# Kernel optimization log

Measured on AMD Instinct MI355X. Metric: run time of the kernel, lower is better.

## Reference

```python
import jax, jax.numpy as jnp
import numpy as np


def setup_inputs() -> dict:
    key = jax.random.key(0)
    k_cb, k_mask, k_y, k_yt, k_ym = jax.random.split(key, 5)
    B, L, M = 8, 2048, 4096
    CB = jax.random.normal(k_cb, (B, L, 3), dtype=jnp.float32) * 10.0
    # residue validity mask: mostly valid, some padding
    mask = (jax.random.uniform(k_mask, (B, L)) > 0.1).astype(jnp.float32)
    Y = jax.random.normal(k_y, (B, M, 3), dtype=jnp.float32) * 10.0
    Y_t = jax.random.randint(k_yt, (B, M), 0, 64, dtype=jnp.int32)
    Y_m = jax.random.randint(k_ym, (B, M), 0, 2, dtype=jnp.int32)
    return {"CB": CB, "mask": mask, "Y": Y, "Y_t": Y_t, "Y_m": Y_m,
            "number_of_ligand_atoms": 25}


def reference(CB, mask, Y, Y_t, Y_m, number_of_ligand_atoms):
    # CB: [B, L, 3], mask: [B, L], Y: [B, M, 3], Y_t/Y_m: [B, M]
    B, L, _ = CB.shape
    k = number_of_ligand_atoms
    Y_m_f = Y_m.astype(jnp.float32)
    mask_CBY = mask[:, :, None] * Y_m_f[:, None, :]          # [B, L, M]
    d = CB[:, :, None, :] - Y[:, None, :, :]                 # [B, L, M, 3]
    L2_AB = jnp.sum(d * d, axis=-1)                          # [B, L, M]
    L2_AB = L2_AB * mask_CBY + (1.0 - mask_CBY) * 1000.0
    # k smallest distances per (b, l); torch uses full argsort + slice,
    # top_k of the negated matrix selects the same set.
    neg_vals, nn_idx = jax.lax.top_k(-L2_AB, k)              # [B, L, k]
    L2_AB_nn = -neg_vals
    D_AB_closest = jnp.sqrt(L2_AB_nn[:, :, 0])               # [B, L]
    b_idx = jnp.arange(B)[:, None, None]                     # [B, 1, 1]
    Y_out = Y[b_idx, nn_idx]                                 # [B, L, k, 3]
    Y_t_out = Y_t[b_idx, nn_idx].astype(jnp.int32)           # [B, L, k]
    Y_m_out = Y_m[b_idx, nn_idx].astype(jnp.int32)           # [B, L, k]
    return Y_out, Y_t_out, Y_m_out, D_AB_closest
```

## Files before the change

kernel.cpp:

```cpp
#include <hip/hip_runtime.h>

#pragma clang fp contract(off)

typedef unsigned long long u64;
typedef unsigned int u32;
typedef unsigned short u16;
typedef float f32x2 __attribute__((ext_vector_type(2)));

#define BB 8
#define LL 2048
#define MM 4096
#define KK 25
#define WPB 16
#define TPB 1024
#define CAP 3072
#define SENT  0xFFFFFFFFFFFFFFFFull
#define SENTH 0xFFFFFFFFu

static __device__ __forceinline__ u32 wave_min_u32(u32 x) {
    u32 t;
    t = (u32)__builtin_amdgcn_update_dpp(0, (int)x, 0xB1, 0xF, 0xF, true);
    x = t < x ? t : x;
    t = (u32)__builtin_amdgcn_update_dpp(0, (int)x, 0x4E, 0xF, 0xF, true);
    x = t < x ? t : x;
    t = (u32)__builtin_amdgcn_update_dpp(0, (int)x, 0x141, 0xF, 0xF, true);
    x = t < x ? t : x;
    t = (u32)__builtin_amdgcn_update_dpp(0, (int)x, 0x140, 0xF, 0xF, true);
    x = t < x ? t : x;
    t = (u32)__builtin_amdgcn_update_dpp((int)x, (int)x, 0x142, 0xF, 0xF, false);
    x = t < x ? t : x;
    t = (u32)__builtin_amdgcn_update_dpp((int)x, (int)x, 0x143, 0xF, 0xF, false);
    x = t < x ? t : x;
    return (u32)__builtin_amdgcn_readlane((int)x, 63);
}

__global__ void __launch_bounds__(TPB, 8) knn_kernel(
    const float* __restrict__ CB, const float* __restrict__ maskA,
    const float* __restrict__ Y, const int* __restrict__ Yt,
    const int* __restrict__ Ym, float* __restrict__ out)
{
    __shared__ __align__(16) float sX[CAP];
    __shared__ __align__(16) float sY[CAP];
    __shared__ __align__(16) float sZ[CAP];
    __shared__ u16 sP16[CAP];
    __shared__ u16 sMidx[64];
    __shared__ int sWinc[16];
    __shared__ int sWbase[16];
    __shared__ int sVtot;
    __shared__ u64 sExt[WPB][64];
    __shared__ u64 sR[WPB][KK];

    const int tid  = threadIdx.x;
    const int lane = tid & 63;
    const int wv   = tid >> 6;
    const int blk  = blockIdx.x;
    const int b    = blk >> 7;
    const int qg   = blk & 127;

    const float* Yb  = Y  + (size_t)b * MM * 3;
    const int*   Ymb = Ym + (size_t)b * MM;
    const int*   Ytb = Yt + (size_t)b * MM;

    const int p0 = tid << 2;
    const float4 f0 = *(const float4*)(Yb + 3 * p0);
    const float4 f1 = *(const float4*)(Yb + 3 * p0 + 4);
    const float4 f2 = *(const float4*)(Yb + 3 * p0 + 8);
    const int4   m4 = *(const int4*)(Ymb + p0);
    const int v0 = (m4.x != 0), v1 = (m4.y != 0), v2 = (m4.z != 0), v3 = (m4.w != 0);
    const int cnt0 = v0 + v1 + v2 + v3;

    int inc = cnt0;
#pragma unroll
    for (int off = 1; off < 64; off <<= 1) {
        const int t = __shfl_up(inc, off, 64);
        if (lane >= off) inc += t;
    }
    if (lane == 63) sWinc[wv] = inc;
    __syncthreads();
    if (tid < 16) {
        const int x = sWinc[tid];
        int ix = x;
#pragma unroll
        for (int off = 1; off < 16; off <<= 1) {
            const int t = __shfl_up(ix, off, 16);
            if (tid >= off) ix += t;
        }
        sWbase[tid] = ix - x;
        if (tid == 15) sVtot = ix;
    }
    __syncthreads();

    {
        int bs = sWbase[wv] + inc - cnt0;
        int mb = p0 - bs;
        if (v0) { sX[bs]=f0.x; sY[bs]=f0.y; sZ[bs]=f0.z; sP16[bs]=(u16)(p0+0); bs++; }
        else    { if (mb < 64) sMidx[mb] = (u16)(p0 + 0); mb++; }
        if (v1) { sX[bs]=f0.w; sY[bs]=f1.x; sZ[bs]=f1.y; sP16[bs]=(u16)(p0+1); bs++; }
        else    { if (mb < 64) sMidx[mb] = (u16)(p0 + 1); mb++; }
        if (v2) { sX[bs]=f1.z; sY[bs]=f1.w; sZ[bs]=f2.x; sP16[bs]=(u16)(p0+2); bs++; }
        else    { if (mb < 64) sMidx[mb] = (u16)(p0 + 2); mb++; }
        if (v3) { sX[bs]=f2.y; sY[bs]=f2.z; sZ[bs]=f2.w; sP16[bs]=(u16)(p0+3); bs++; }
        else    { if (mb < 64) sMidx[mb] = (u16)(p0 + 3); mb++; }
    }
    const int V  = sVtot;
    const int NJ = (V + 255) >> 8;
    for (int c = V + tid; c < (NJ << 8); c += TPB) {
        sX[c] = __builtin_inff(); sY[c] = 0.0f; sZ[c] = 0.0f; sP16[c] = 4095;
    }
    __syncthreads();

    const int l = qg * WPB + wv;
    const int q = b * LL + l;

    float* out_y = out;
    float* out_t = out + (size_t)BB * LL * KK * 3;
    float* out_m = out_t + (size_t)BB * LL * KK;
    float* out_d = out_m + (size_t)BB * LL * KK;

    if (maskA[q] == 0.0f) {
        if (lane < KK) {
            const int p = lane;
            const size_t o = (size_t)q * KK + lane;
            out_y[3 * o + 0] = Yb[3 * p + 0];
            out_y[3 * o + 1] = Yb[3 * p + 1];
            out_y[3 * o + 2] = Yb[3 * p + 2];
            out_t[o] = (float)Ytb[p];
            out_m[o] = (float)Ymb[p];
            if (lane == 0) out_d[q] = sqrtf(1000.0f);
        }
        return;
    }

    const float cx = CB[3 * q + 0];
    const float cy = CB[3 * q + 1];
    const float cz = CB[3 * q + 2];

    float v1f = 3.0e38f, v2f = 3.0e38f, v3f = 3.0e38f, v4f = 3.0e38f;
    u32 J = 0u;
    const u32 SEL1 = 0x06050400u;
    const u32 SEL2 = 0x06050004u;
    const u32 SEL3 = 0x06000504u;
    const u32 SEL4 = 0x00060504u;
    auto ins = [&](float v, u32 id) {
        const bool c1 = v < v1f, c2 = v < v2f, c3 = v < v3f, c4 = v < v4f;
        const u32 sel = c1 ? SEL1 : (c2 ? SEL2 : (c3 ? SEL3 : SEL4));
        const u32 Jp  = __builtin_amdgcn_perm(J, id, sel);
        const float n2 = __builtin_amdgcn_fmed3f(v, v1f, v2f);
        const float n3 = __builtin_amdgcn_fmed3f(v, v2f, v3f);
        const float n4 = __builtin_amdgcn_fmed3f(v, v3f, v4f);
        v1f = fminf(v, v1f);
        v2f = n2; v3f = n3; v4f = n4;
        J = c4 ? Jp : J;
    };

    const f32x2 cxx = {cx, cx}, cyy = {cy, cy}, czz = {cz, cz};
#pragma unroll 2
    for (int j = 0; j < NJ; ++j) {
        const int base = (j << 8) + (lane << 2);
        const float4 xq = *(const float4*)&sX[base];
        const float4 yq = *(const float4*)&sY[base];
        const float4 zq = *(const float4*)&sZ[base];
        f32x2 dx = cxx - f32x2{xq.x, xq.y};
        f32x2 dy = cyy - f32x2{yq.x, yq.y};
        f32x2 dz = czz - f32x2{zq.x, zq.y};
        const f32x2 d01 = (dx * dx + dy * dy) + dz * dz;
        dx = cxx - f32x2{xq.z, xq.w};
        dy = cyy - f32x2{yq.z, yq.w};
        dz = czz - f32x2{zq.z, zq.w};
        const f32x2 d23 = (dx * dx + dy * dy) + dz * dz;
        ins(d01.x, (u32)(j << 2));
        ins(d01.y, (u32)((j << 2) | 1));
        ins(d23.x, (u32)((j << 2) | 2));
        ins(d23.y, (u32)((j << 2) | 3));
    }

    auto slotof = [&](u32 id) -> u32 {
        return ((id >> 2) << 8) | (u32)(lane << 2) | (id & 3u);
    };

    const u32 s1 = slotof( J        & 0xFFu);
    const u32 s2 = slotof((J >>  8) & 0xFFu);
    const u32 s3 = slotof((J >> 16) & 0xFFu);
    const u32 s4 = slotof((J >> 24) & 0xFFu);
    u32 h1 = __float_as_uint(v1f) + 1u;
    u32 h2 = __float_as_uint(v2f) + 1u;
    u32 h3 = __float_as_uint(v3f) + 1u;
    u32 h4 = __float_as_uint(v4f) + 1u;
    u64 lref = ((u64)h4 << 32) | s4;

    bool fb = false;
    u64 myk = 0;
    {
        const u32 T = wave_min_u32(h4);
        const bool c1 = (h1 <= T), c2 = (h2 <= T), c3 = (h3 <= T), c4 = (h4 <= T);
        const u64 b1 = __ballot(c1), b2 = __ballot(c2);
        const u64 b3 = __ballot(c3), b4 = __ballot(c4);
        const int n1 = __popcll(b1), n2 = __popcll(b2), n3 = __popcll(b3);
        const int total = n1 + n2 + n3 + __popcll(b4);
        if (total > 64) {
            fb = true;
        } else {
            const u64 below = (1ull << lane) - 1ull;
            u64* sE = sExt[wv];
            sE[lane] = SENT;
            if (lane == 24) sR[wv][24] = SENT;
            int pos = __popcll(b1 & below);
            if (c1) sE[pos] = ((u64)h1 << 32) | s1;
            pos = n1 + __popcll(b2 & below);
            if (c2) sE[pos] = ((u64)h2 << 32) | s2;
            pos = n1 + n2 + __popcll(b3 & below);
            if (c3) sE[pos] = ((u64)h3 << 32) | s3;
            pos = n1 + n2 + n3 + __popcll(b4 & below);
            if (c4) sE[pos] = ((u64)h4 << 32) | s4;
            const u64 mk = sE[lane];
            int rank = 0;
            const int tot = (total + 7) & ~7;
#pragma unroll 8
            for (int i = 0; i < tot; ++i)
                rank += (sE[i] < mk) ? 1 : 0;
            if (rank < KK && mk != SENT) sR[wv][rank] = mk;
            const u64 K25 = sR[wv][24];
            if (__any(lref < K25)) fb = true;
            else if (lane < KK) myk = sR[wv][lane];
        }
    }

    if (fb) {
#pragma unroll 1
        for (int it = 0; it < KK; ++it) {
            if (it >= 4 && __any(h1 == SENTH)) {
                const bool need = (h1 == SENTH);
                u64 found = SENT;
                const int NI = NJ << 2;
#pragma unroll 4
                for (int id = 0; id < NI; ++id) {
                    const u32 s = slotof((u32)id);
                    const float dx = cx - sX[s];
                    const float dy = cy - sY[s];
                    const float dz = cz - sZ[s];
                    const float v = (dx * dx + dy * dy) + dz * dz;
                    const u64 key = ((u64)(__float_as_uint(v) + 1u) << 32) | s;
                    if (key > lref && key < found) found = key;
                }
                if (need) {
                    const u32 s = (u32)found & 0xFFFFu;
                    h1 = (u32)(found >> 32);
                    J = (J & ~0xFFu) | (((s >> 8) << 2) | (s & 3u));
                    lref = found;
                }
            }
            const u32 bv = wave_min_u32(h1);
            const u64 ball = __ballot(h1 == bv);
            bool win = (h1 == bv);
            if (__popcll(ball) != 1) {
                const u32 vl = slotof(J & 0xFFu);
                u32 cp = win ? vl : 0xFFFFFFFFu;
#pragma unroll
                for (int off = 32; off; off >>= 1) {
                    const u32 o = __shfl_xor(cp, off, 64);
                    cp = (o < cp) ? o : cp;
                }
                win = win && (vl == cp);
            }
            if (win) {
                sExt[wv][it] = ((u64)h1 << 32) | slotof(J & 0xFFu);
                h1 = h2; h2 = h3; h3 = h4; h4 = SENTH;
                J >>= 8;
            }
        }
        if (lane < KK) myk = sExt[wv][lane];
    }

    const u32 mvh   = (u32)(myk >> 32);
    const u32 mslot = (u32)myk & 0xFFFFu;
    const bool less = (lane < KK) && (mvh < 0x447A0001u);
    const int nless = __popcll(__ballot(less));
    if (lane < KK) {
        int p; float val, mflag;
        if (lane < nless) {
            p = (int)sP16[mslot];
            val = __uint_as_float(mvh - 1u);
            mflag = 1.0f;
        } else {
            p = (int)sMidx[lane - nless];
            val = 1000.0f;
            mflag = 0.0f;
        }
        const size_t o = (size_t)q * KK + lane;
        out_y[3 * o + 0] = Yb[3 * p + 0];
        out_y[3 * o + 1] = Yb[3 * p + 1];
        out_y[3 * o + 2] = Yb[3 * p + 2];
        out_t[o] = (float)Ytb[p];
        out_m[o] = mflag;
        if (lane == 0) out_d[q] = sqrtf(val);
    }
}

extern "C" void kernel_launch(void* const* d_in, const int* in_sizes, int n_in,
                              void* d_out, int out_size, void* d_ws, size_t ws_size,
                              hipStream_t stream) {
    const float* CB   = (const float*)d_in[0];
    const float* mask = (const float*)d_in[1];
    const float* Y    = (const float*)d_in[2];
    const int*   Yt   = (const int*)d_in[3];
    const int*   Ym   = (const int*)d_in[4];
    float* out = (float*)d_out;

    dim3 grid(BB * LL / WPB);
    dim3 block(TPB);
    hipLaunchKernelGGL(knn_kernel, grid, block, 0, stream, CB, mask, Y, Yt, Ym, out);
}
```

Before: 103.7 us.

## Add second-round refill to wave top-k merge before full fallback

Grows the per-wave candidate buffer from 64 to 96 entries and ranks two candidates per lane. When a lane's four held candidates may not cover the global 25th key, that lane rescans its shared-memory points for the next four keys above its last one and appends them. The merge is then recomputed, so the slow 25-iteration fallback runs less often. This adds shared memory, a divergent rescan by a few lanes, and a second merge pass.

```diff
diff --git a/kernel.cpp b/kernel.cpp
--- a/kernel.cpp
+++ b/kernel.cpp
@@ -14,6 +14,7 @@
 #define WPB 16
 #define TPB 1024
 #define CAP 3072
+#define ECAP 96
 #define SENT  0xFFFFFFFFFFFFFFFFull
 #define SENTH 0xFFFFFFFFu
 
@@ -47,7 +48,7 @@
     __shared__ int sWinc[16];
     __shared__ int sWbase[16];
     __shared__ int sVtot;
-    __shared__ u64 sExt[WPB][64];
+    __shared__ u64 sExt[WPB][ECAP];
     __shared__ u64 sR[WPB][KK];
 
     const int tid  = threadIdx.x;
@@ -197,12 +198,13 @@
         const u64 b3 = __ballot(c3), b4 = __ballot(c4);
         const int n1 = __popcll(b1), n2 = __popcll(b2), n3 = __popcll(b3);
         const int total = n1 + n2 + n3 + __popcll(b4);
-        if (total > 64) {
+        if (total > ECAP) {
             fb = true;
         } else {
             const u64 below = (1ull << lane) - 1ull;
             u64* sE = sExt[wv];
             sE[lane] = SENT;
+            if (lane < ECAP - 64) sE[64 + lane] = SENT;
             if (lane == 24) sR[wv][24] = SENT;
             int pos = __popcll(b1 & below);
             if (c1) sE[pos] = ((u64)h1 << 32) | s1;
@@ -212,16 +214,74 @@
             if (c3) sE[pos] = ((u64)h3 << 32) | s3;
             pos = n1 + n2 + n3 + __popcll(b4 & below);
             if (c4) sE[pos] = ((u64)h4 << 32) | s4;
-            const u64 mk = sE[lane];
-            int rank = 0;
-            const int tot = (total + 7) & ~7;
+            u64 mk0 = sE[lane];
+            u64 mk1 = (lane < ECAP - 64) ? sE[64 + lane] : SENT;
+            int rank0 = 0, rank1 = 0;
+            int tot = (total + 7) & ~7;
 #pragma unroll 8
-            for (int i = 0; i < tot; ++i)
-                rank += (sE[i] < mk) ? 1 : 0;
-            if (rank < KK && mk != SENT) sR[wv][rank] = mk;
-            const u64 K25 = sR[wv][24];
-            if (__any(lref < K25)) fb = true;
-            else if (lane < KK) myk = sR[wv][lane];
+            for (int i = 0; i < tot; ++i) {
+                const u64 e = sE[i];
+                rank0 += (e < mk0) ? 1 : 0;
+                rank1 += (e < mk1) ? 1 : 0;
+            }
+            if (mk0 != SENT && rank0 < KK) sR[wv][rank0] = mk0;
+            if (mk1 != SENT && rank1 < KK) sR[wv][rank1] = mk1;
+            u64 K25 = sR[wv][24];
+            const bool need = (lref < K25);
+            if (__any(need)) {
+                u64 r1k = SENT, r2k = SENT, r3k = SENT, r4k = SENT;
+                if (need) {
+                    const int NI = NJ << 2;
+#pragma unroll 2
+                    for (int id = 0; id < NI; ++id) {
+                        const u32 s = slotof((u32)id);
+                        const float dx = cx - sX[s];
+                        const float dy = cy - sY[s];
+                        const float dz = cz - sZ[s];
+                        const float v = (dx * dx + dy * dy) + dz * dz;
+                        u64 key = ((u64)(__float_as_uint(v) + 1u) << 32) | s;
+                        key = (key > lref) ? key : SENT;
+                        const bool d1 = key < r1k, d2 = key < r2k,
+                                   d3 = key < r3k, d4 = key < r4k;
+                        const u64 m4k = d4 ? (d3 ? r3k : key) : r4k;
+                        const u64 m3k = d3 ? (d2 ? r2k : key) : r3k;
+                        const u64 m2k = d2 ? (d1 ? r1k : key) : r2k;
+                        const u64 m1k = d1 ? key : r1k;
+                        r1k = m1k; r2k = m2k; r3k = m3k; r4k = m4k;
+                    }
+                }
+                const u64 nb = __ballot(need);
+                const int newtot = total + 4 * __popcll(nb);
+                if (newtot > ECAP) {
+                    fb = true;
+                } else {
+                    if (need) {
+                        const int bpos = total + 4 * __popcll(nb & below);
+                        sE[bpos + 0] = r1k;
+                        sE[bpos + 1] = r2k;
+                        sE[bpos + 2] = r3k;
+                        sE[bpos + 3] = r4k;
+                    }
+                    mk0 = sE[lane];
+                    mk1 = (lane < ECAP - 64) ? sE[64 + lane] : SENT;
+                    rank0 = 0; rank1 = 0;
+                    tot = (newtot + 7) & ~7;
+#pragma unroll 8
+                    for (int i = 0; i < tot; ++i) {
+                        const u64 e = sE[i];
+                        rank0 += (e < mk0) ? 1 : 0;
+                        rank1 += (e < mk1) ? 1 : 0;
+                    }
+                    if (mk0 != SENT && rank0 < KK) sR[wv][rank0] = mk0;
+                    if (mk1 != SENT && rank1 < KK) sR[wv][rank1] = mk1;
+                    K25 = sR[wv][24];
+                    const u64 le = need ? r4k : lref;
+                    if (__any(le < K25)) fb = true;
+                    else if (lane < KK) myk = sR[wv][lane];
+                }
+            } else {
+                if (lane < KK) myk = sR[wv][lane];
+            }
         }
     }
 
```

New measurement: 114.9 us. 10.8% more time.
